# Optimization experiments

Measured on AMD Instinct MI355X. Metric: run time of the kernel, lower is better.

Reference implementation:

```python
import jax, jax.numpy as jnp
import numpy as np

N = 50000        # num_nodes
E = 800000       # num edges (avg degree 16)
IN = 512         # embedding_dim[0]
H = 128          # hidden_dim = embedding_dim[1]
C = 64           # out_dim = n_classes = embedding_dim[-1]
L = 3            # layer_num = len(embedding_dim) - 1


def _lin(k, fan_in, fan_out):
    s = 1.0 / np.sqrt(fan_in)
    k1, k2 = jax.random.split(k)
    W = jax.random.uniform(k1, (fan_in, fan_out), jnp.float32, -s, s)
    b = jax.random.uniform(k2, (fan_out,), jnp.float32, -s, s)
    return W, b


def setup_inputs() -> dict:
    key = jax.random.key(0)
    ks = jax.random.split(key, 12)
    d = {}
    d["x"] = jax.random.normal(ks[0], (N, IN), jnp.float32)
    d["edge_index"] = jax.random.randint(ks[1], (2, E), 0, N)
    # pseudo_mlp: in_dim -> 512 -> 64 -> out_dim
    d["Wp1"], d["bp1"] = _lin(ks[2], IN, 512)
    d["Wp2"], d["bp2"] = _lin(ks[3], 512, 64)
    d["Wp3"], d["bp3"] = _lin(ks[4], 64, C)
    # parsing_mats[0] (only ln=0 is used in learn_soft_edge3), init ones/scaling_factor
    d["parsing0"] = jnp.ones((C, C), jnp.float32) / 2.0 + 0.01 * jax.random.normal(ks[5], (C, C), jnp.float32)
    # GCNConv weights (PyG style: linear without bias, bias added after aggregation)
    d["Wg0"], d["bg0"] = _lin(ks[6], IN, H)
    d["Wg1"], d["bg1"] = _lin(ks[7], H, H)
    d["Wg2"], d["bg2"] = _lin(ks[8], H, H)
    # JK 'cat' -> lin1 input is (layer_num-1)*hidden
    d["Wl1"], d["bl1"] = _lin(ks[9], (L - 1) * H, H)
    d["Wl2"], d["bl2"] = _lin(ks[10], H, C)
    return d


def gcn_conv(x, W, b, edge_index, ew, n):
    """PyG GCNConv with per-edge weight ew, add_self_loops=True (loop weight 1)."""
    xw = x @ W                                           # [N, F_out]
    row, col = edge_index[0], edge_index[1]
    loop = jnp.arange(n)
    row2 = jnp.concatenate([row, loop])
    col2 = jnp.concatenate([col, loop])
    ew2 = jnp.concatenate([ew, jnp.ones((n,), xw.dtype)])
    deg = jax.ops.segment_sum(ew2, col2, num_segments=n)
    dis = jnp.where(deg > 0, jax.lax.rsqrt(deg), 0.0)    # deg^-1/2, inf -> 0
    norm = dis[row2] * ew2 * dis[col2]                   # [E+N]
    out = jax.ops.segment_sum(norm[:, None] * xw[row2], col2, num_segments=n)
    return out + b


def soft_edge_weight(x, edge_index, Wp1, bp1, Wp2, bp2, Wp3, bp3, parsing0):
    """learn_soft_edge3: bilinear form start^T * relu(2*P) * end per edge.
    Original materializes an [E,C,C] outer product then bmm + diagonal; the
    diagonal-sum equals einsum('ek,ed,dk->e', start, end, parsing), computed
    here as a fused small matmul + elementwise reduce (same math)."""
    h = jax.nn.relu(x @ Wp1 + bp1)
    h = jax.nn.relu(h @ Wp2 + bp2)
    logits = h @ Wp3 + bp3                               # [N, C]
    parsing = jax.nn.relu(2.0 * parsing0)                # scaling_factor = 2
    s = logits[edge_index[0]]                            # [E, C] start
    e = logits[edge_index[1]]                            # [E, C] end
    ew = jnp.sum((e @ parsing) * s, axis=-1)             # [E]
    mean = ew.mean()
    var = jnp.var(ew, ddof=1)                            # torch .var() is unbiased
    return (ew - mean) * jnp.sqrt(1e-4 / var) + 1.0


def reference(x, edge_index, Wp1, bp1, Wp2, bp2, Wp3, bp3, parsing0,
              Wg0, bg0, Wg1, bg1, Wg2, bg2, Wl1, bl1, Wl2, bl2):
    n = x.shape[0]
    ew = soft_edge_weight(x, edge_index, Wp1, bp1, Wp2, bp2, Wp3, bp3, parsing0)
    # layer 0
    x1 = jax.nn.relu(gcn_conv(x, Wg0, bg0, edge_index, ew, n))
    xs = [x1]
    # ln = 1 (not last): conv -> relu -> (dropout off in eval) -> append
    x2 = jax.nn.relu(gcn_conv(x1, Wg1, bg1, edge_index, ew, n))
    xs.append(x2)
    # ln = 2 (last layer): computed in original but loop breaks before append;
    # jump(xs) overwrites x, so the last conv's output never reaches the output.
    xj = jnp.concatenate(xs, axis=-1)                    # JK 'cat' -> [N, (L-1)*H]
    out = jax.nn.relu(xj @ Wl1 + bl1)
    out = out @ Wl2 + bl2                                # [N, C]
    return out
```

## Files before the change

### kernel.cpp

```cpp
#include <hip/hip_runtime.h>
#include <hip/hip_bf16.h>
#include <cmath>
#include <cstring>

#define NNODES 50000
#define NEDGES 800000
#define IND    512
#define HD     128
#define CD     64

typedef __bf16 bf16x8 __attribute__((ext_vector_type(8)));
typedef float  f32x4  __attribute__((ext_vector_type(4)));
typedef const __attribute__((address_space(1))) unsigned int* gu32p;
typedef __attribute__((address_space(3))) unsigned int* lu32p;

static const size_t XB_B   = 0;
static const size_t XJ_B   = 0;
static const size_t HID_B  = 25600000;
static const size_t H1_B   = 51200000;
static const size_t XW_B   = 102400000;
static const size_t H2_B   = 115200000;
static const size_t LG_B   = 121600000;
static const size_t PE_B   = 128000000;
static const size_t WT_B   = 134400000;
static const size_t CSRR_B = 135300000;
static const size_t EWC_B  = 138500000;
static const size_t CSRW_B = 141700000;
static const size_t CNT_B  = 144900000;
static const size_t S_B    = 145100000;
static const size_t ZERO_BYTES = 200016;
static const size_t RP_B   = 145100016;
static const size_t WOFF_B = 145300020;
static const size_t INCL_B = 145500020;
static const size_t BSUM_B = 145700020;
static const size_t ST_B   = 145701044;
static const size_t DIS_B  = 145701052;

static const size_t WP1T_O = 0;
static const size_t WG0T_O = 524288;
static const size_t WP2T_O = 655360;
static const size_t WP3T_O = 720896;
static const size_t W2T_O  = 729088;
static const size_t WG1T_O = 737280;
static const size_t WL1T_O = 770048;
static const size_t WL2T_O = 835584;
static const size_t BG1_O  = 851968;
static const size_t BG3_O  = 854528;

struct WD { const float* s; __hip_bfloat16* d; int K; int N; };
struct WP { WD w[7]; };

__global__ __launch_bounds__(256) void transpose_cast_all(WP p)
{
    WD d = p.w[blockIdx.y];
    int i = blockIdx.x * 256 + threadIdx.x;
    if (i >= d.K * d.N) return;
    int k = i % d.K, n = i / d.K;
    d.d[i] = __float2bfloat16(d.s[(size_t)k * d.N + n]);
}

__global__ __launch_bounds__(256) void combine_p0(
    const float* __restrict__ Wp3, const float* __restrict__ bp3,
    const float* __restrict__ P0, const float* __restrict__ bp1,
    __hip_bfloat16* __restrict__ W2t, float* __restrict__ bias_g1,
    float* __restrict__ bias_g3)
{
    int b = blockIdx.x;
    if (b < 16) {
        int i = b * 256 + threadIdx.x;
        int k = i >> 6, n = i & 63;
        float s = 0.f;
        for (int j = 0; j < 64; j++)
            s += Wp3[k * 64 + j] * fmaxf(2.f * P0[j * 64 + n], 0.f);
        W2t[n * 64 + k] = __float2bfloat16(s);
    } else if (b == 16) {
        int n = threadIdx.x;
        if (n < 64) {
            float s = 0.f;
            for (int j = 0; j < 64; j++)
                s += bp3[j] * fmaxf(2.f * P0[j * 64 + n], 0.f);
            bias_g3[n] = bp3[n];
            bias_g3[64 + n] = s;
        }
    } else {
        int i = (b - 17) * 256 + threadIdx.x;
        if (i < 512) bias_g1[i] = bp1[i];
        else if (i < 640) bias_g1[i] = 0.f;
    }
}

__global__ __launch_bounds__(256) void cast_x_kernel(
    const float* __restrict__ x, __hip_bfloat16* __restrict__ xb, long n)
{
    long i = ((long)blockIdx.x * 256 + threadIdx.x) * 8;
    if (i >= n) return;
    float4 a = *(const float4*)(x + i);
    float4 b = *(const float4*)(x + i + 4);
    __hip_bfloat16 o[8] __attribute__((aligned(16)));
    o[0] = __float2bfloat16(a.x); o[1] = __float2bfloat16(a.y);
    o[2] = __float2bfloat16(a.z); o[3] = __float2bfloat16(a.w);
    o[4] = __float2bfloat16(b.x); o[5] = __float2bfloat16(b.y);
    o[6] = __float2bfloat16(b.z); o[7] = __float2bfloat16(b.w);
    *(int4*)(xb + i) = *(const int4*)o;
}

template<int BN, int WN>
__global__ __launch_bounds__(256) void gemm_mfma(
    const __hip_bfloat16* __restrict__ A, int lda,
    const __hip_bfloat16* __restrict__ Bt, int ldb,
    const float* __restrict__ bias,
    void* __restrict__ Cout, int ldc,
    void* __restrict__ Cout2, int ldc2, int splitN,
    int M, int K, int do_relu, int out_bf16)
{
    constexpr int BF = WN / 16;
    constexpr int BPASS = BN / 64;
    __shared__ __bf16 As[128 * 32];
    __shared__ __bf16 Bs[BN * 32];

    const int NC = gridDim.x, NR = gridDim.y;
    int g = blockIdx.y * NC + blockIdx.x;
    int per = NC * 8;
    int nfull = (NR >> 3) * per;
    int rowt, colt;
    if (g < nfull) {
        int grp = g / per, rem = g % per;
        rowt = grp * 8 + (rem & 7);
        colt = rem >> 3;
    } else {
        int rem = g - nfull;
        int tail = NR - (NR >> 3) * 8;
        rowt = (NR >> 3) * 8 + rem % tail;
        colt = rem / tail;
    }

    const int t = threadIdx.x;
    const int row0 = rowt * 128;
    const int col0 = colt * BN;

    const int wv   = t >> 6;
    const int lane = t & 63;
    const int quad = lane >> 4;
    const int l16  = lane & 15;
    const int wrow = (wv >> 1) * 64;
    const int wcol = (wv & 1) * WN;

    const int subrow = lane >> 2;
    const int subkg  = (lane & 3) * 8;

    f32x4 acc[4][BF] = {};

    for (int k0 = 0; k0 < K; k0 += 32) {
        #pragma unroll
        for (int p = 0; p < 2; p++) {
            int rowA = (p * 4 + wv) * 16 + subrow;
            const __hip_bfloat16* gp = A + (size_t)(row0 + rowA) * lda + k0 + subkg;
            __builtin_amdgcn_global_load_lds((gu32p)(const void*)gp,
                (lu32p)(void*)&As[(p * 4 + wv) * 512], 16, 0, 0);
        }
        #pragma unroll
        for (int p = 0; p < BPASS; p++) {
            int rowB = (p * 4 + wv) * 16 + subrow;
            const __hip_bfloat16* gp = Bt + (size_t)(col0 + rowB) * ldb + k0 + subkg;
            __builtin_amdgcn_global_load_lds((gu32p)(const void*)gp,
                (lu32p)(void*)&Bs[(p * 4 + wv) * 512], 16, 0, 0);
        }
        __syncthreads();

        bf16x8 af[4], bfr[BF];
        #pragma unroll
        for (int i = 0; i < 4; i++)
            af[i] = *(const bf16x8*)&As[(wrow + i * 16 + l16) * 32 + quad * 8];
        #pragma unroll
        for (int j = 0; j < BF; j++)
            bfr[j] = *(const bf16x8*)&Bs[(wcol + j * 16 + l16) * 32 + quad * 8];
        #pragma unroll
        for (int i = 0; i < 4; i++)
            #pragma unroll
            for (int j = 0; j < BF; j++)
                acc[i][j] = __builtin_amdgcn_mfma_f32_16x16x32_bf16(af[i], bfr[j], acc[i][j], 0, 0, 0);
        __syncthreads();
    }

    #pragma unroll
    for (int i = 0; i < 4; i++) {
        #pragma unroll
        for (int j = 0; j < BF; j++) {
            int n = col0 + wcol + j * 16 + l16;
            bool second = (n >= splitN);
            float bv = bias ? bias[n] : 0.f;
            #pragma unroll
            for (int reg = 0; reg < 4; reg++) {
                int m = row0 + wrow + i * 16 + quad * 4 + reg;
                if (m >= M) continue;
                float v = acc[i][j][reg] + bv;
                if (do_relu && !second) v = fmaxf(v, 0.f);
                if (second)
                    ((__hip_bfloat16*)Cout2)[(size_t)m * ldc2 + (n - splitN)] = __float2bfloat16(v);
                else if (out_bf16)
                    ((__hip_bfloat16*)Cout)[(size_t)m * ldc + n] = __float2bfloat16(v);
                else
                    ((float*)Cout)[(size_t)m * ldc + n] = v;
            }
        }
    }
}

__global__ __launch_bounds__(256) void count_kernel(
    const int* __restrict__ ei, int* __restrict__ cnt)
{
    int e = blockIdx.x * 256 + threadIdx.x;
    if (e >= NEDGES) return;
    atomicAdd(&cnt[ei[NEDGES + e]], 1);
}

__global__ __launch_bounds__(256) void scan1_kernel(
    const int* __restrict__ cnt, int* __restrict__ incl, int* __restrict__ bsum)
{
    __shared__ int s[256];
    int t = threadIdx.x;
    int i = blockIdx.x * 256 + t;
    int v = (i < NNODES) ? cnt[i] : 0;
    s[t] = v;
    __syncthreads();
    for (int off = 1; off < 256; off <<= 1) {
        int u = (t >= off) ? s[t - off] : 0;
        __syncthreads();
        s[t] += u;
        __syncthreads();
    }
    if (i < NNODES) incl[i] = s[t];
    if (t == 255) bsum[blockIdx.x] = s[255];
}

__global__ __launch_bounds__(256) void scan2_kernel(int* __restrict__ bsum, int nb)
{
    __shared__ int s[256];
    int t = threadIdx.x;
    int v = (t < nb) ? bsum[t] : 0;
    s[t] = v;
    __syncthreads();
    for (int off = 1; off < 256; off <<= 1) {
        int u = (t >= off) ? s[t - off] : 0;
        __syncthreads();
        s[t] += u;
        __syncthreads();
    }
    if (t < nb) bsum[t] = s[t] - v;
}

__global__ __launch_bounds__(256) void scan3_kernel(
    const int* __restrict__ cnt, const int* __restrict__ incl,
    const int* __restrict__ bsum, int* __restrict__ rowptr, int* __restrict__ woff)
{
    int i = blockIdx.x * 256 + threadIdx.x;
    if (i >= NNODES) return;
    int off = bsum[blockIdx.x];
    int r = incl[i] - cnt[i] + off;
    rowptr[i] = r;
    woff[i] = r;
    if (i == NNODES - 1) rowptr[NNODES] = incl[i] + off;
}

__global__ __launch_bounds__(256) void scatter_idx_kernel(
    const int* __restrict__ ei, int* __restrict__ woff,
    int* __restrict__ csr_row, int* __restrict__ csr_col)
{
    int e = blockIdx.x * 256 + threadIdx.x;
    if (e >= NEDGES) return;
    int r = ei[e];
    int c = ei[NEDGES + e];
    int p = atomicAdd(&woff[c], 1);
    csr_row[p] = r;
    csr_col[p] = c;
}

__global__ __launch_bounds__(256) void edge_ew_gather(
    const __hip_bfloat16* __restrict__ lg, const __hip_bfloat16* __restrict__ pe,
    const int* __restrict__ csr_row, const int* __restrict__ csr_col,
    float* __restrict__ ew_csr)
{
    const int tid = threadIdx.x;
    const int sub = tid & 7;
    const int e = blockIdx.x * 32 + (tid >> 3);
    if (e >= NEDGES) return;
    int r = csr_row[e];
    int c = csr_col[e];
    bf16x8 a = *(const bf16x8*)(lg + (size_t)r * CD + sub * 8);
    bf16x8 b = *(const bf16x8*)(pe + (size_t)c * CD + sub * 8);
    float acc = 0.f;
    #pragma unroll
    for (int u = 0; u < 8; u++)
        acc += (float)a[u] * (float)b[u];
    acc += __shfl_xor(acc, 1);
    acc += __shfl_xor(acc, 2);
    acc += __shfl_xor(acc, 4);
    if (sub == 0) ew_csr[e] = acc;
}

__global__ __launch_bounds__(256) void ew_stats_kernel(
    const float* __restrict__ ew, double* __restrict__ S)
{
    const int tid = threadIdx.x;
    double s1 = 0.0, s2 = 0.0;
    for (int i = blockIdx.x * 256 + tid; i < NEDGES; i += gridDim.x * 256) {
        float v = ew[i];
        s1 += v; s2 += (double)v * (double)v;
    }
    __shared__ double sh1[256], sh2[256];
    sh1[tid] = s1; sh2[tid] = s2;
    __syncthreads();
    for (int s = 128; s > 0; s >>= 1) {
        if (tid < s) { sh1[tid] += sh1[tid + s]; sh2[tid] += sh2[tid + s]; }
        __syncthreads();
    }
    if (tid == 0) {
        atomicAdd(&S[0], sh1[0]);
        atomicAdd(&S[1], sh2[0]);
    }
}

__global__ void stats_kernel(const double* __restrict__ S, float* __restrict__ st)
{
    double E = (double)NEDGES;
    double mean = S[0] / E;
    double var = (S[1] - S[0] * S[0] / E) / (E - 1.0);
    st[0] = (float)mean;
    st[1] = (float)sqrt(1e-4 / var);
}

__global__ __launch_bounds__(256) void norm_deg_kernel(
    const int* __restrict__ rowptr, float* __restrict__ ew_csr,
    const float* __restrict__ st, float* __restrict__ dis)
{
    int n = blockIdx.x * 256 + threadIdx.x;
    if (n >= NNODES) return;
    float mean = st[0], alpha = st[1];
    int s = rowptr[n], e = rowptr[n + 1];
    float sum = 0.f;
    for (int j = s; j < e; j++) {
        float w = (ew_csr[j] - mean) * alpha + 1.0f;
        ew_csr[j] = w;
        sum += w;
    }
    float d = sum + 1.0f;
    dis[n] = (d > 0.f) ? rsqrtf(d) : 0.f;
}

__global__ __launch_bounds__(256) void csrw_kernel(
    const int* __restrict__ rowptr, const int* __restrict__ csr_row,
    const float* __restrict__ ew_csr, const float* __restrict__ dis,
    float* __restrict__ csr_w)
{
    int n = blockIdx.x * 256 + threadIdx.x;
    if (n >= NNODES) return;
    float dn = dis[n];
    int s = rowptr[n], e = rowptr[n + 1];
    for (int j = s; j < e; j++)
        csr_w[j] = dis[csr_row[j]] * ew_csr[j] * dn;
}

__global__ __launch_bounds__(128) void agg_kernel(
    const unsigned* __restrict__ xw32, const float* __restrict__ dis,
    const int* __restrict__ rowptr, const int* __restrict__ csr_row,
    const float* __restrict__ csr_w, const float* __restrict__ bias,
    __hip_bfloat16* __restrict__ out, int ldo)
{
    const int wv = threadIdx.x >> 6, lane = threadIdx.x & 63;
    const int n = blockIdx.x * 2 + wv;
    if (n >= NNODES) return;
    float dn = dis[n];
    unsigned v0 = xw32[(size_t)n * 64 + lane];
    float aL = dn * dn * __uint_as_float(v0 << 16);
    float aH = dn * dn * __uint_as_float(v0 & 0xffff0000u);
    int s = rowptr[n], e = rowptr[n + 1];
    int j = s;
    for (; j + 4 <= e; j += 4) {
        int r0 = csr_row[j], r1 = csr_row[j + 1];
        int r2 = csr_row[j + 2], r3 = csr_row[j + 3];
        float w0 = csr_w[j], w1 = csr_w[j + 1];
        float w2 = csr_w[j + 2], w3 = csr_w[j + 3];
        unsigned g0 = xw32[(size_t)r0 * 64 + lane];
        unsigned g1 = xw32[(size_t)r1 * 64 + lane];
        unsigned g2 = xw32[(size_t)r2 * 64 + lane];
        unsigned g3 = xw32[(size_t)r3 * 64 + lane];
        aL = fmaf(w0, __uint_as_float(g0 << 16), aL);
        aH = fmaf(w0, __uint_as_float(g0 & 0xffff0000u), aH);
        aL = fmaf(w1, __uint_as_float(g1 << 16), aL);
        aH = fmaf(w1, __uint_as_float(g1 & 0xffff0000u), aH);
        aL = fmaf(w2, __uint_as_float(g2 << 16), aL);
        aH = fmaf(w2, __uint_as_float(g2 & 0xffff0000u), aH);
        aL = fmaf(w3, __uint_as_float(g3 << 16), aL);
        aH = fmaf(w3, __uint_as_float(g3 & 0xffff0000u), aH);
    }
    for (; j < e; j++) {
        int r = csr_row[j];
        float w = csr_w[j];
        unsigned g = xw32[(size_t)r * 64 + lane];
        aL = fmaf(w, __uint_as_float(g << 16), aL);
        aH = fmaf(w, __uint_as_float(g & 0xffff0000u), aH);
    }
    float2 b = *(const float2*)(bias + 2 * lane);
    aL = fmaxf(aL + b.x, 0.f);
    aH = fmaxf(aH + b.y, 0.f);
    __hip_bfloat16 bl = __float2bfloat16(aL), bh = __float2bfloat16(aH);
    unsigned short ul, uh;
    memcpy(&ul, &bl, 2); memcpy(&uh, &bh, 2);
    unsigned o = (unsigned)ul | ((unsigned)uh << 16);
    *(unsigned*)(out + (size_t)n * ldo + 2 * lane) = o;
}

extern "C" void kernel_launch(void* const* d_in, const int* in_sizes, int n_in,
                              void* d_out, int out_size, void* d_ws, size_t ws_size,
                              hipStream_t stream)
{
    const float* x   = (const float*)d_in[0];
    const int*   ei  = (const int*)d_in[1];
    const float* Wp1 = (const float*)d_in[2];
    const float* bp1 = (const float*)d_in[3];
    const float* Wp2 = (const float*)d_in[4];
    const float* bp2 = (const float*)d_in[5];
    const float* Wp3 = (const float*)d_in[6];
    const float* bp3 = (const float*)d_in[7];
    const float* P0  = (const float*)d_in[8];
    const float* Wg0 = (const float*)d_in[9];
    const float* bg0 = (const float*)d_in[10];
    const float* Wg1 = (const float*)d_in[11];
    const float* bg1 = (const float*)d_in[12];
    const float* Wl1 = (const float*)d_in[15];
    const float* bl1 = (const float*)d_in[16];
    const float* Wl2 = (const float*)d_in[17];
    const float* bl2 = (const float*)d_in[18];
    float* out = (float*)d_out;

    char* wsb = (char*)d_ws;
    __hip_bfloat16* xb     = (__hip_bfloat16*)(wsb + XB_B);
    __hip_bfloat16* xj     = (__hip_bfloat16*)(wsb + XJ_B);
    __hip_bfloat16* hid    = (__hip_bfloat16*)(wsb + HID_B);
    __hip_bfloat16* h1     = (__hip_bfloat16*)(wsb + H1_B);
    __hip_bfloat16* xw     = (__hip_bfloat16*)(wsb + XW_B);
    __hip_bfloat16* h2     = (__hip_bfloat16*)(wsb + H2_B);
    __hip_bfloat16* lg     = (__hip_bfloat16*)(wsb + LG_B);
    __hip_bfloat16* pe     = (__hip_bfloat16*)(wsb + PE_B);
    int*            csr_row= (int*)(wsb + CSRR_B);
    float*          ew_csr = (float*)(wsb + EWC_B);
    int*            csr_col= (int*)(wsb + CSRW_B);
    float*          csr_w  = (float*)(wsb + CSRW_B);
    int*            cnt    = (int*)(wsb + CNT_B);
    double*         S      = (double*)(wsb + S_B);
    int*            rowptr = (int*)(wsb + RP_B);
    int*            woff   = (int*)(wsb + WOFF_B);
    int*            incl   = (int*)(wsb + INCL_B);
    int*            bsum   = (int*)(wsb + BSUM_B);
    float*          st     = (float*)(wsb + ST_B);
    float*          dis    = (float*)(wsb + DIS_B);

    __hip_bfloat16* Wp1t = (__hip_bfloat16*)(wsb + WT_B + WP1T_O);
    __hip_bfloat16* Wg0t = (__hip_bfloat16*)(wsb + WT_B + WG0T_O);
    __hip_bfloat16* Wp2t = (__hip_bfloat16*)(wsb + WT_B + WP2T_O);
    __hip_bfloat16* Wp3t = (__hip_bfloat16*)(wsb + WT_B + WP3T_O);
    __hip_bfloat16* W2t  = (__hip_bfloat16*)(wsb + WT_B + W2T_O);
    __hip_bfloat16* Wg1t = (__hip_bfloat16*)(wsb + WT_B + WG1T_O);
    __hip_bfloat16* Wl1t = (__hip_bfloat16*)(wsb + WT_B + WL1T_O);
    __hip_bfloat16* Wl2t = (__hip_bfloat16*)(wsb + WT_B + WL2T_O);
    float*          bias_g1 = (float*)(wsb + WT_B + BG1_O);
    float*          bias_g3 = (float*)(wsb + WT_B + BG3_O);

    const int EB = (NEDGES + 255) / 256;
    const int NB = (NNODES + 255) / 256;
    const int MT = (NNODES + 127) / 128;
    const int BIGN = 1 << 30;

    hipMemsetAsync(wsb + CNT_B, 0, ZERO_BYTES, stream);

    WP wp;
    wp.w[0] = { Wp1, Wp1t, 512, 512 };
    wp.w[1] = { Wg0, Wg0t, 512, 128 };
    wp.w[2] = { Wp2, Wp2t, 512,  64 };
    wp.w[3] = { Wp3, Wp3t,  64,  64 };
    wp.w[4] = { Wg1, Wg1t, 128, 128 };
    wp.w[5] = { Wl1, Wl1t, 256, 128 };
    wp.w[6] = { Wl2, Wl2t, 128,  64 };
    transpose_cast_all<<<dim3(1024, 7), 256, 0, stream>>>(wp);
    combine_p0<<<20, 256, 0, stream>>>(Wp3, bp3, P0, bp1, W2t, bias_g1, bias_g3);
    cast_x_kernel<<<12500, 256, 0, stream>>>(x, xb, (long)NNODES * IND);

    count_kernel<<<EB, 256, 0, stream>>>(ei, cnt);
    scan1_kernel<<<NB, 256, 0, stream>>>(cnt, incl, bsum);
    scan2_kernel<<<1, 256, 0, stream>>>(bsum, NB);
    scan3_kernel<<<NB, 256, 0, stream>>>(cnt, incl, bsum, rowptr, woff);
    scatter_idx_kernel<<<EB, 256, 0, stream>>>(ei, woff, csr_row, csr_col);

    gemm_mfma<128, 64><<<dim3(5, MT), 256, 0, stream>>>(
        xb, 512, Wp1t, 512, bias_g1, h1, 512, xw, 128, 512, NNODES, 512, 1, 1);

    gemm_mfma<64, 32><<<dim3(1, MT), 256, 0, stream>>>(
        h1, 512, Wp2t, 512, bp2, h2, 64, nullptr, 0, BIGN, NNODES, 512, 1, 1);

    gemm_mfma<128, 64><<<dim3(1, MT), 256, 0, stream>>>(
        h2, 64, Wp3t, 64, bias_g3, lg, 64, pe, 64, 64, NNODES, 64, 0, 1);

    edge_ew_gather<<<(NEDGES + 31) / 32, 256, 0, stream>>>(lg, pe, csr_row, csr_col, ew_csr);
    ew_stats_kernel<<<512, 256, 0, stream>>>(ew_csr, S);
    stats_kernel<<<1, 1, 0, stream>>>(S, st);
    norm_deg_kernel<<<NB, 256, 0, stream>>>(rowptr, ew_csr, st, dis);
    csrw_kernel<<<NB, 256, 0, stream>>>(rowptr, csr_row, ew_csr, dis, csr_w);

    agg_kernel<<<25000, 128, 0, stream>>>((const unsigned*)xw, dis, rowptr, csr_row, csr_w, bg0, xj, 2 * HD);

    gemm_mfma<64, 32><<<dim3(2, MT), 256, 0, stream>>>(
        xj, 2 * HD, Wg1t, 128, nullptr, xw, 128, nullptr, 0, BIGN, NNODES, 128, 0, 1);
    agg_kernel<<<25000, 128, 0, stream>>>((const unsigned*)xw, dis, rowptr, csr_row, csr_w, bg1, xj + HD, 2 * HD);

    gemm_mfma<128, 64><<<dim3(1, MT), 256, 0, stream>>>(
        xj, 2 * HD, Wl1t, 256, bl1, hid, 128, nullptr, 0, BIGN, NNODES, 256, 1, 1);
    gemm_mfma<64, 32><<<dim3(1, MT), 256, 0, stream>>>(
        hid, 128, Wl2t, 128, bl2, out, 64, nullptr, 0, BIGN, NNODES, 128, 0, 0);
}
```

Before: 576.6 us.

## Fuse fp32-to-bf16 cast of x into first GEMM and swizzle LDS tiles

Removes the separate pass that converted x to bf16. The first GEMM now loads fp32 x directly, converts in registers, and stores to a padded LDS tile. Separately, the LDS layout for the async-loaded tiles gets an XOR swizzle to reduce bank conflicts on fragment reads. The trade-off is that the fused GEMM reads twice the bytes for A with synchronous loads, and these are repeated across column tiles.

```diff
diff --git a/kernel.cpp b/kernel.cpp
--- a/kernel.cpp
+++ b/kernel.cpp
@@ -14,7 +14,6 @@
 typedef const __attribute__((address_space(1))) unsigned int* gu32p;
 typedef __attribute__((address_space(3))) unsigned int* lu32p;
 
-static const size_t XB_B   = 0;
 static const size_t XJ_B   = 0;
 static const size_t HID_B  = 25600000;
 static const size_t H1_B   = 51200000;
@@ -89,24 +88,9 @@
     }
 }
 
-__global__ __launch_bounds__(256) void cast_x_kernel(
-    const float* __restrict__ x, __hip_bfloat16* __restrict__ xb, long n)
-{
-    long i = ((long)blockIdx.x * 256 + threadIdx.x) * 8;
-    if (i >= n) return;
-    float4 a = *(const float4*)(x + i);
-    float4 b = *(const float4*)(x + i + 4);
-    __hip_bfloat16 o[8] __attribute__((aligned(16)));
-    o[0] = __float2bfloat16(a.x); o[1] = __float2bfloat16(a.y);
-    o[2] = __float2bfloat16(a.z); o[3] = __float2bfloat16(a.w);
-    o[4] = __float2bfloat16(b.x); o[5] = __float2bfloat16(b.y);
-    o[6] = __float2bfloat16(b.z); o[7] = __float2bfloat16(b.w);
-    *(int4*)(xb + i) = *(const int4*)o;
-}
-
-template<int BN, int WN>
+template<int BN, int WN, int CAST_A>
 __global__ __launch_bounds__(256) void gemm_mfma(
-    const __hip_bfloat16* __restrict__ A, int lda,
+    const void* __restrict__ Ap, int lda,
     const __hip_bfloat16* __restrict__ Bt, int ldb,
     const float* __restrict__ bias,
     void* __restrict__ Cout, int ldc,
@@ -115,7 +99,8 @@
 {
     constexpr int BF = WN / 16;
     constexpr int BPASS = BN / 64;
-    __shared__ __bf16 As[128 * 32];
+    constexpr int AST = CAST_A ? 40 : 32;
+    __shared__ __bf16 As[128 * AST];
     __shared__ __bf16 Bs[BN * 32];
 
     const int NC = gridDim.x, NR = gridDim.y;
@@ -146,17 +131,35 @@
     const int wcol = (wv & 1) * WN;
 
     const int subrow = lane >> 2;
-    const int subkg  = (lane & 3) * 8;
+    const int kchunk = (lane & 3) ^ (subrow & 3);
+    const int subkg  = kchunk * 8;
 
     f32x4 acc[4][BF] = {};
 
     for (int k0 = 0; k0 < K; k0 += 32) {
-        #pragma unroll
-        for (int p = 0; p < 2; p++) {
-            int rowA = (p * 4 + wv) * 16 + subrow;
-            const __hip_bfloat16* gp = A + (size_t)(row0 + rowA) * lda + k0 + subkg;
-            __builtin_amdgcn_global_load_lds((gu32p)(const void*)gp,
-                (lu32p)(void*)&As[(p * 4 + wv) * 512], 16, 0, 0);
+        if (CAST_A) {
+            const float* Af = (const float*)Ap;
+            #pragma unroll
+            for (int p = 0; p < 4; p++) {
+                int idx = t + p * 256;
+                int r = idx >> 3, kg = (idx & 7) * 4;
+                int m = row0 + r;
+                if (m > M - 1) m = M - 1;
+                float4 v = *(const float4*)(Af + (size_t)m * lda + k0 + kg);
+                __hip_bfloat16 o[4] __attribute__((aligned(8)));
+                o[0] = __float2bfloat16(v.x); o[1] = __float2bfloat16(v.y);
+                o[2] = __float2bfloat16(v.z); o[3] = __float2bfloat16(v.w);
+                *(int2*)&As[r * AST + kg] = *(const int2*)o;
+            }
+        } else {
+            const __hip_bfloat16* Ab = (const __hip_bfloat16*)Ap;
+            #pragma unroll
+            for (int p = 0; p < 2; p++) {
+                int rowA = (p * 4 + wv) * 16 + subrow;
+                const __hip_bfloat16* gp = Ab + (size_t)(row0 + rowA) * lda + k0 + subkg;
+                __builtin_amdgcn_global_load_lds((gu32p)(const void*)gp,
+                    (lu32p)(void*)&As[(p * 4 + wv) * 512], 16, 0, 0);
+            }
         }
         #pragma unroll
         for (int p = 0; p < BPASS; p++) {
@@ -169,11 +172,16 @@
 
         bf16x8 af[4], bfr[BF];
         #pragma unroll
-        for (int i = 0; i < 4; i++)
-            af[i] = *(const bf16x8*)&As[(wrow + i * 16 + l16) * 32 + quad * 8];
+        for (int i = 0; i < 4; i++) {
+            int R = wrow + i * 16 + l16;
+            int c = CAST_A ? quad : (quad ^ (R & 3));
+            af[i] = *(const bf16x8*)&As[R * AST + c * 8];
+        }
         #pragma unroll
-        for (int j = 0; j < BF; j++)
-            bfr[j] = *(const bf16x8*)&Bs[(wcol + j * 16 + l16) * 32 + quad * 8];
+        for (int j = 0; j < BF; j++) {
+            int R = wcol + j * 16 + l16;
+            bfr[j] = *(const bf16x8*)&Bs[R * 32 + (quad ^ (R & 3)) * 8];
+        }
         #pragma unroll
         for (int i = 0; i < 4; i++)
             #pragma unroll
@@ -434,7 +442,6 @@
     float* out = (float*)d_out;
 
     char* wsb = (char*)d_ws;
-    __hip_bfloat16* xb     = (__hip_bfloat16*)(wsb + XB_B);
     __hip_bfloat16* xj     = (__hip_bfloat16*)(wsb + XJ_B);
     __hip_bfloat16* hid    = (__hip_bfloat16*)(wsb + HID_B);
     __hip_bfloat16* h1     = (__hip_bfloat16*)(wsb + H1_B);
@@ -483,7 +490,6 @@
     wp.w[6] = { Wl2, Wl2t, 128,  64 };
     transpose_cast_all<<<dim3(1024, 7), 256, 0, stream>>>(wp);
     combine_p0<<<20, 256, 0, stream>>>(Wp3, bp3, P0, bp1, W2t, bias_g1, bias_g3);
-    cast_x_kernel<<<12500, 256, 0, stream>>>(x, xb, (long)NNODES * IND);
 
     count_kernel<<<EB, 256, 0, stream>>>(ei, cnt);
     scan1_kernel<<<NB, 256, 0, stream>>>(cnt, incl, bsum);
@@ -491,13 +497,13 @@
     scan3_kernel<<<NB, 256, 0, stream>>>(cnt, incl, bsum, rowptr, woff);
     scatter_idx_kernel<<<EB, 256, 0, stream>>>(ei, woff, csr_row, csr_col);
 
-    gemm_mfma<128, 64><<<dim3(5, MT), 256, 0, stream>>>(
-        xb, 512, Wp1t, 512, bias_g1, h1, 512, xw, 128, 512, NNODES, 512, 1, 1);
-
-    gemm_mfma<64, 32><<<dim3(1, MT), 256, 0, stream>>>(
+    gemm_mfma<128, 64, 1><<<dim3(5, MT), 256, 0, stream>>>(
+        x, 512, Wp1t, 512, bias_g1, h1, 512, xw, 128, 512, NNODES, 512, 1, 1);
+
+    gemm_mfma<64, 32, 0><<<dim3(1, MT), 256, 0, stream>>>(
         h1, 512, Wp2t, 512, bp2, h2, 64, nullptr, 0, BIGN, NNODES, 512, 1, 1);
 
-    gemm_mfma<128, 64><<<dim3(1, MT), 256, 0, stream>>>(
+    gemm_mfma<128, 64, 0><<<dim3(1, MT), 256, 0, stream>>>(
         h2, 64, Wp3t, 64, bias_g3, lg, 64, pe, 64, 64, NNODES, 64, 0, 1);
 
     edge_ew_gather<<<(NEDGES + 31) / 32, 256, 0, stream>>>(lg, pe, csr_row, csr_col, ew_csr);
@@ -508,12 +514,12 @@
 
     agg_kernel<<<25000, 128, 0, stream>>>((const unsigned*)xw, dis, rowptr, csr_row, csr_w, bg0, xj, 2 * HD);
 
-    gemm_mfma<64, 32><<<dim3(2, MT), 256, 0, stream>>>(
+    gemm_mfma<64, 32, 0><<<dim3(2, MT), 256, 0, stream>>>(
         xj, 2 * HD, Wg1t, 128, nullptr, xw, 128, nullptr, 0, BIGN, NNODES, 128, 0, 1);
     agg_kernel<<<25000, 128, 0, stream>>>((const unsigned*)xw, dis, rowptr, csr_row, csr_w, bg1, xj + HD, 2 * HD);
 
-    gemm_mfma<128, 64><<<dim3(1, MT), 256, 0, stream>>>(
+    gemm_mfma<128, 64, 0><<<dim3(1, MT), 256, 0, stream>>>(
         xj, 2 * HD, Wl1t, 256, bl1, hid, 128, nullptr, 0, BIGN, NNODES, 256, 1, 1);
-    gemm_mfma<64, 32><<<dim3(1, MT), 256, 0, stream>>>(
+    gemm_mfma<64, 32, 0><<<dim3(1, MT), 256, 0, stream>>>(
         hid, 128, Wl2t, 128, bl2, out, 64, nullptr, 0, BIGN, NNODES, 128, 0, 0);
 }
```

After: 573.3 us. About the same (-0.6%).
